# Optimization experiments

Measured on AMD Instinct MI355X. Metric: run time of the kernel, lower is better.

## Reference

```python
import jax, jax.numpy as jnp
import numpy as np

D_MODEL = 1024
N_HEADS = 16
D_HEAD = D_MODEL // N_HEADS
D_FF = 4096
EPS = 1e-5
NEG = -1e10


def setup_inputs() -> dict:
    key = jax.random.key(0)
    ks = jax.random.split(key, 16)
    s = 0.02
    x = jax.random.normal(ks[0], (4, 1024, D_MODEL), dtype=jnp.float32)
    mask = jnp.ones((4, 1, 1, 1024), dtype=jnp.int32)
    return {
        "x": x,
        "mask": mask,
        "Wq": jax.random.normal(ks[1], (D_MODEL, D_MODEL), jnp.float32) * s,
        "Wk": jax.random.normal(ks[2], (D_MODEL, D_MODEL), jnp.float32) * s,
        "Wv": jax.random.normal(ks[3], (D_MODEL, D_MODEL), jnp.float32) * s,
        "Wp": jax.random.normal(ks[4], (D_MODEL, D_MODEL), jnp.float32) * s,
        "bp": jnp.zeros((D_MODEL,), jnp.float32),
        "W1": jax.random.normal(ks[5], (D_MODEL, D_FF), jnp.float32) * s,
        "b1": jnp.zeros((D_FF,), jnp.float32),
        "W2": jax.random.normal(ks[6], (D_FF, D_MODEL), jnp.float32) * s,
        "b2": jnp.zeros((D_MODEL,), jnp.float32),
        "g1": jnp.ones((D_MODEL,), jnp.float32),
        "be1": jnp.zeros((D_MODEL,), jnp.float32),
        "g2": jnp.ones((D_MODEL,), jnp.float32),
        "be2": jnp.zeros((D_MODEL,), jnp.float32),
    }


def _layer_norm(x, g, b):
    mu = jnp.mean(x, axis=-1, keepdims=True)
    var = jnp.mean(jnp.square(x - mu), axis=-1, keepdims=True)
    return (x - mu) * jax.lax.rsqrt(var + EPS) * g + b


def _mha(x, mask, Wq, Wk, Wv, Wp, bp):
    B, L, _ = x.shape
    q = (x @ Wq).reshape(B, L, N_HEADS, D_HEAD).transpose(0, 2, 1, 3)  # (B,H,L,dh)
    k = (x @ Wk).reshape(B, L, N_HEADS, D_HEAD).transpose(0, 2, 1, 3)
    v = (x @ Wv).reshape(B, L, N_HEADS, D_HEAD).transpose(0, 2, 1, 3)
    scores = jnp.einsum('bhqd,bhkd->bhqk', q, k) / jnp.sqrt(jnp.float32(D_HEAD))
    scores = jnp.where(mask == 0, NEG, scores)
    attn = jax.nn.softmax(scores, axis=-1)
    heads = jnp.einsum('bhqk,bhkd->bhqd', attn, v)  # (B,H,L,dh)
    heads = heads.transpose(0, 2, 1, 3).reshape(B, L, D_MODEL)
    return heads @ Wp + bp


def reference(x, mask, Wq, Wk, Wv, Wp, bp, W1, b1, W2, b2, g1, be1, g2, be2):
    # Post-norm residual sublayers (dropout inactive at inference)
    attn_out = _mha(x, mask, Wq, Wk, Wv, Wp, bp)
    h = _layer_norm(x + attn_out, g1, be1)
    ff = jax.nn.relu(h @ W1 + b1) @ W2 + b2
    out = _layer_norm(h + ff, g2, be2)
    return out
```

## Files before the change

kernel.cpp:

```cpp
#include <hip/hip_runtime.h>
#include <hip/hip_bf16.h>

typedef __attribute__((ext_vector_type(8))) short short8;
typedef __attribute__((ext_vector_type(4))) short short4v;
typedef __attribute__((ext_vector_type(4))) float float4v;

static __device__ __forceinline__ float b2f(short s) {
    return __builtin_bit_cast(float, ((unsigned)(unsigned short)s) << 16);
}
static __device__ __forceinline__ short f2b(float f) {
    unsigned x = __builtin_bit_cast(unsigned, f);
    unsigned r = (x + 0x7fffu + ((x >> 16) & 1u)) >> 16;
    return (short)r;
}
static __device__ __forceinline__ void gload_lds16(const short* g, short* l) {
    __builtin_amdgcn_global_load_lds(
        (const __attribute__((address_space(1))) void*)g,
        (__attribute__((address_space(3))) void*)l, 16, 0, 0);
}

__global__ __launch_bounds__(256) void cvt_k(const float* __restrict__ in,
                                             short* __restrict__ out)
{
    const size_t i = ((size_t)blockIdx.x * 256 + threadIdx.x) * 4;
    const float4v v = *(const float4v*)&in[i];
    short4v s;
#pragma unroll
    for (int j = 0; j < 4; j++) s[j] = f2b(v[j]);
    *(short4v*)&out[i] = s;
}

__global__ __launch_bounds__(256) void transpose_cvt_k(const float* __restrict__ in,
                                                       short* __restrict__ out,
                                                       int R, int C)
{
    __shared__ float tile[64][65];
    const int tx = threadIdx.x;
    const int r0 = blockIdx.y * 64, c0 = blockIdx.x * 64;
    const int lr = tx >> 4, lc = (tx & 15) * 4;
#pragma unroll
    for (int p = 0; p < 4; p++) {
        const float4v v = *(const float4v*)&in[(size_t)(r0 + lr + p * 16) * C + c0 + lc];
#pragma unroll
        for (int j = 0; j < 4; j++) tile[lr + p * 16][lc + j] = v[j];
    }
    __syncthreads();
    const int oc = tx >> 3, orr = (tx & 7) * 8;
#pragma unroll
    for (int p = 0; p < 2; p++) {
        const int c = oc + p * 32;
        short8 pk;
#pragma unroll
        for (int j = 0; j < 8; j++) pk[j] = f2b(tile[orr + j][c]);
        *(short8*)&out[(size_t)(c0 + c) * R + r0 + orr] = pk;
    }
}

#define BK 32
template<int MODE, int BM>
__global__ __launch_bounds__(256) void gemm_bt(const short* __restrict__ X,
                                               const short* __restrict__ Wt,
                                               short* __restrict__ out,
                                               const float* __restrict__ bias,
                                               const short* __restrict__ res,
                                               int M, int N, int K)
{
    constexpr int MI = BM / 32;
    constexpr int WM = BM / 2;
    __shared__ short As[BM * BK];
    __shared__ short Bs[128 * BK];
    const int tid = threadIdx.x;
    const int wave = tid >> 6, lane = tid & 63;
    const int quad = lane >> 4, l16 = lane & 15;
    const int m0 = blockIdx.y * BM, n0 = blockIdx.x * 128;
    const int wm = (wave >> 1) * WM, wn = (wave & 1) * 64;

    const int srow = tid >> 2, scol = (tid & 3) * 8;
    const short* gA0 = X  + (size_t)(m0 + srow) * K + scol;
    const short* gA1 = X  + (size_t)(m0 + srow + 64) * K + scol;
    const short* gB0 = Wt + (size_t)(n0 + srow) * K + scol;
    const short* gB1 = Wt + (size_t)(n0 + srow + 64) * K + scol;
    short* lA0 = As + tid * 8;
    short* lA1 = As + (tid + 256) * 8;
    short* lB0 = Bs + tid * 8;
    short* lB1 = Bs + (tid + 256) * 8;

    float4v acc[MI][4] = {};

    for (int k0 = 0; k0 < K; k0 += BK) {
        gload_lds16(gA0 + k0, lA0);
        if (BM == 128) gload_lds16(gA1 + k0, lA1);
        gload_lds16(gB0 + k0, lB0);
        gload_lds16(gB1 + k0, lB1);
        __syncthreads();
        short8 af[MI], bfr[4];
#pragma unroll
        for (int i = 0; i < MI; i++) af[i]  = *(const short8*)&As[(wm + i * 16 + l16) * BK + quad * 8];
#pragma unroll
        for (int i = 0; i < 4; i++)  bfr[i] = *(const short8*)&Bs[(wn + i * 16 + l16) * BK + quad * 8];
#pragma unroll
        for (int mi = 0; mi < MI; mi++)
#pragma unroll
            for (int ni = 0; ni < 4; ni++)
                acc[mi][ni] = __builtin_amdgcn_mfma_f32_16x16x32_bf16(af[mi], bfr[ni], acc[mi][ni], 0, 0, 0);
        __syncthreads();
    }

#pragma unroll
    for (int mi = 0; mi < MI; mi++) {
#pragma unroll
        for (int ni = 0; ni < 4; ni++) {
            const int gn = n0 + wn + ni * 16 + l16;
            const float bv = (MODE == 2 || MODE == 3) ? bias[gn] : 0.0f;
#pragma unroll
            for (int r = 0; r < 4; r++) {
                const int gm = m0 + wm + mi * 16 + quad * 4 + r;
                float v = acc[mi][ni][r];
                if (MODE == 4) {
                    const int s = gn >> 10;
                    const int n = gn & 1023;
                    const int hh = n >> 6, d = n & 63;
                    const size_t bh16 = (size_t)((gm >> 10) * 16 + hh) << 16;
                    const size_t base = (size_t)s << 22;
                    if (s == 0)      out[base + bh16 + ((size_t)(gm & 1023) << 6) + d] = f2b(v * 0.125f);
                    else if (s == 1) out[base + bh16 + ((size_t)(gm & 1023) << 6) + d] = f2b(v);
                    else             out[base + bh16 + ((size_t)d << 10) + (gm & 1023)] = f2b(v);
                } else if (MODE == 2) {
                    v += bv;
                    v = fmaxf(v, 0.0f);
                    out[(size_t)gm * N + gn] = f2b(v);
                } else {
                    v += bv + b2f(res[(size_t)gm * N + gn]);
                    out[(size_t)gm * N + gn] = f2b(v);
                }
            }
        }
    }
}

__global__ __launch_bounds__(256) void attn_k(const short* __restrict__ Qb,
                                              const short* __restrict__ Kb,
                                              const short* __restrict__ Vt,
                                              const int* __restrict__ mask,
                                              short* __restrict__ heads)
{
    __shared__ short Kl[2][64 * 32];
    __shared__ short Vl[2][64 * 32];
    __shared__ short P[4][16 * 72];
    const int bh = blockIdx.x, qb = blockIdx.y;
    const int b = bh >> 4, h = bh & 15;
    const int tid = threadIdx.x, wave = tid >> 6, lane = tid & 63;
    const int quad = lane >> 4, l16 = lane & 15;
    const int qbase = qb * 64 + wave * 16;
    const short* Qp = Qb + ((size_t)bh << 16) + (size_t)qbase * 64;
    const short* Kp = Kb + ((size_t)bh << 16);
    const short* Vp = Vt + ((size_t)bh << 16);
    const int* mp = mask + (b << 10);

    const short8 bq0 = *(const short8*)&Qp[l16 * 64 + quad * 8];
    const short8 bq1 = *(const short8*)&Qp[l16 * 64 + 32 + quad * 8];

    float rs = 0.0f;
    float4v o[4] = {};
    short* myP = &P[wave][0];

    const int srow = tid >> 2, sc8 = (tid & 3) * 8;

    for (int kc = 0; kc < 1024; kc += 64) {
        gload_lds16(Kp + (size_t)(kc + srow) * 64 + sc8,      &Kl[0][tid * 8]);
        gload_lds16(Kp + (size_t)(kc + srow) * 64 + 32 + sc8, &Kl[1][tid * 8]);
        gload_lds16(Vp + (size_t)srow * 1024 + kc + sc8,      &Vl[0][tid * 8]);
        gload_lds16(Vp + (size_t)srow * 1024 + kc + 32 + sc8, &Vl[1][tid * 8]);
        __syncthreads();

        float4v s[4];
#pragma unroll
        for (int kt = 0; kt < 4; kt++) {
            s[kt] = (float4v){};
            const short8 ka = *(const short8*)&Kl[0][(kt * 16 + l16) * 32 + quad * 8];
            s[kt] = __builtin_amdgcn_mfma_f32_16x16x32_bf16(ka, bq0, s[kt], 0, 0, 0);
            const short8 kb = *(const short8*)&Kl[1][(kt * 16 + l16) * 32 + quad * 8];
            s[kt] = __builtin_amdgcn_mfma_f32_16x16x32_bf16(kb, bq1, s[kt], 0, 0, 0);
        }
#pragma unroll
        for (int kt = 0; kt < 4; kt++) {
            const int4 mv = *(const int4*)&mp[kc + kt * 16 + quad * 4];
            float p0 = mv.x ? __expf(fminf(s[kt][0], 30.f)) : 0.f;
            float p1 = mv.y ? __expf(fminf(s[kt][1], 30.f)) : 0.f;
            float p2 = mv.z ? __expf(fminf(s[kt][2], 30.f)) : 0.f;
            float p3 = mv.w ? __expf(fminf(s[kt][3], 30.f)) : 0.f;
            rs += (p0 + p1) + (p2 + p3);
            short4v w;
            w[0] = f2b(p0); w[1] = f2b(p1); w[2] = f2b(p2); w[3] = f2b(p3);
            *(short4v*)&myP[l16 * 72 + kt * 16 + quad * 4] = w;
        }
        const short8 bp0 = *(const short8*)&myP[l16 * 72 + quad * 8];
        const short8 bp1 = *(const short8*)&myP[l16 * 72 + 32 + quad * 8];
#pragma unroll
        for (int dt = 0; dt < 4; dt++) {
            const short8 va = *(const short8*)&Vl[0][(dt * 16 + l16) * 32 + quad * 8];
            o[dt] = __builtin_amdgcn_mfma_f32_16x16x32_bf16(va, bp0, o[dt], 0, 0, 0);
            const short8 vb = *(const short8*)&Vl[1][(dt * 16 + l16) * 32 + quad * 8];
            o[dt] = __builtin_amdgcn_mfma_f32_16x16x32_bf16(vb, bp1, o[dt], 0, 0, 0);
        }
        __syncthreads();
    }

    rs += __shfl_xor(rs, 16);
    rs += __shfl_xor(rs, 32);
    const float inv = 1.0f / fmaxf(rs, 1e-20f);
    const int gq = qbase + l16;
#pragma unroll
    for (int dt = 0; dt < 4; dt++) {
        short4v w;
#pragma unroll
        for (int r = 0; r < 4; r++) w[r] = f2b(o[dt][r] * inv);
        *(short4v*)&heads[((size_t)(b * 1024 + gq) << 10) + h * 64 + dt * 16 + quad * 4] = w;
    }
}

template<bool F32OUT>
__global__ __launch_bounds__(256) void ln_k(const short* __restrict__ in,
                                            const float* __restrict__ g,
                                            const float* __restrict__ be,
                                            short* __restrict__ outb,
                                            float* __restrict__ outf)
{
    __shared__ float red[8];
    const int row = blockIdx.x, tid = threadIdx.x;
    const short* p = in + ((size_t)row << 10);
    float v[4];
#pragma unroll
    for (int i = 0; i < 4; i++) v[i] = b2f(p[tid + i * 256]);
    float s = v[0] + v[1] + v[2] + v[3];
#pragma unroll
    for (int off = 32; off; off >>= 1) s += __shfl_xor(s, off);
    if ((tid & 63) == 0) red[tid >> 6] = s;
    __syncthreads();
    const float mu = (red[0] + red[1] + red[2] + red[3]) * (1.0f / 1024.0f);
    float vs = 0.f;
#pragma unroll
    for (int i = 0; i < 4; i++) { const float d = v[i] - mu; vs += d * d; }
#pragma unroll
    for (int off = 32; off; off >>= 1) vs += __shfl_xor(vs, off);
    if ((tid & 63) == 0) red[4 + (tid >> 6)] = vs;
    __syncthreads();
    const float rstd = rsqrtf((red[4] + red[5] + red[6] + red[7]) * (1.0f / 1024.0f) + 1e-5f);
#pragma unroll
    for (int i = 0; i < 4; i++) {
        const int c = tid + i * 256;
        const float r = (v[i] - mu) * rstd * g[c] + be[c];
        if (F32OUT) outf[((size_t)row << 10) + c] = r;
        else        outb[((size_t)row << 10) + c] = f2b(r);
    }
}

extern "C" void kernel_launch(void* const* d_in, const int* in_sizes, int n_in,
                              void* d_out, int out_size, void* d_ws, size_t ws_size,
                              hipStream_t stream)
{
    const float* x   = (const float*)d_in[0];
    const int*   mk  = (const int*)d_in[1];
    const float* Wq  = (const float*)d_in[2];
    const float* Wk  = (const float*)d_in[3];
    const float* Wv  = (const float*)d_in[4];
    const float* Wp  = (const float*)d_in[5];
    const float* bp  = (const float*)d_in[6];
    const float* W1  = (const float*)d_in[7];
    const float* b1  = (const float*)d_in[8];
    const float* W2  = (const float*)d_in[9];
    const float* b2  = (const float*)d_in[10];
    const float* g1  = (const float*)d_in[11];
    const float* be1 = (const float*)d_in[12];
    const float* g2  = (const float*)d_in[13];
    const float* be2 = (const float*)d_in[14];
    float* out = (float*)d_out;

    char* ws = (char*)d_ws;
    const size_t MB = (size_t)1 << 20;
    short* xb     = (short*)(ws + 0 * MB);
    short* WqkvT  = (short*)(ws + 8 * MB);
    short* WpT    = (short*)(ws + 14 * MB);
    short* W1T    = (short*)(ws + 16 * MB);
    short* W2T    = (short*)(ws + 24 * MB);
    short* Qb     = (short*)(ws + 32 * MB);
    short* Kb     = (short*)(ws + 40 * MB);
    short* Vt     = (short*)(ws + 48 * MB);
    short* hd     = (short*)(ws + 56 * MB);
    short* u      = (short*)(ws + 32 * MB);
    short* hpre   = (short*)(ws + 64 * MB);
    short* hbuf   = (short*)(ws + 72 * MB);

    const dim3 blk(256);

    cvt_k<<<dim3(4096), blk, 0, stream>>>(x, xb);

    transpose_cvt_k<<<dim3(16, 16), blk, 0, stream>>>(Wq, WqkvT, 1024, 1024);
    transpose_cvt_k<<<dim3(16, 16), blk, 0, stream>>>(Wk, WqkvT + (1 << 20), 1024, 1024);
    transpose_cvt_k<<<dim3(16, 16), blk, 0, stream>>>(Wv, WqkvT + (2 << 20), 1024, 1024);
    transpose_cvt_k<<<dim3(16, 16), blk, 0, stream>>>(Wp, WpT, 1024, 1024);
    transpose_cvt_k<<<dim3(64, 16), blk, 0, stream>>>(W1, W1T, 1024, 4096);
    transpose_cvt_k<<<dim3(16, 64), blk, 0, stream>>>(W2, W2T, 4096, 1024);

    gemm_bt<4, 128><<<dim3(24, 32), blk, 0, stream>>>(xb, WqkvT, Qb, nullptr, nullptr, 4096, 3072, 1024);

    attn_k<<<dim3(64, 16), blk, 0, stream>>>(Qb, Kb, Vt, mk, hd);

    gemm_bt<3, 64><<<dim3(8, 64), blk, 0, stream>>>(hd, WpT, hpre, bp, xb, 4096, 1024, 1024);

    ln_k<false><<<dim3(4096), blk, 0, stream>>>(hpre, g1, be1, hbuf, nullptr);

    gemm_bt<2, 128><<<dim3(32, 32), blk, 0, stream>>>(hbuf, W1T, u, b1, nullptr, 4096, 4096, 1024);

    gemm_bt<3, 64><<<dim3(8, 64), blk, 0, stream>>>(u, W2T, hpre, b2, hbuf, 4096, 1024, 4096);

    ln_k<true><<<dim3(4096), blk, 0, stream>>>(hpre, g2, be2, nullptr, out);
}
```

Baseline: 383.9 us.

## Double the GEMM K-step to 64 and add a BN template parameter

The GEMM main loop now loads a 64-wide K slice per iteration into two 32-wide LDS halves. This halves the number of barrier pairs and loop iterations and gives more MFMA work between syncs. A BN template parameter is added, and the two N=1024 GEMMs switch to 64x64 tiles with twice as many blocks to improve occupancy and CU fill. The cost is more LDS per block and a smaller tile size with less reuse for those two GEMMs.

```diff
diff --git a/kernel.cpp b/kernel.cpp
--- a/kernel.cpp
+++ b/kernel.cpp
@@ -56,8 +56,7 @@
     }
 }
 
-#define BK 32
-template<int MODE, int BM>
+template<int MODE, int BM, int BN>
 __global__ __launch_bounds__(256) void gemm_bt(const short* __restrict__ X,
                                                const short* __restrict__ Wt,
                                                short* __restrict__ out,
@@ -65,51 +64,53 @@
                                                const short* __restrict__ res,
                                                int M, int N, int K)
 {
-    constexpr int MI = BM / 32;
-    constexpr int WM = BM / 2;
-    __shared__ short As[BM * BK];
-    __shared__ short Bs[128 * BK];
+    constexpr int MI = BM / 32, NI = BN / 32;
+    __shared__ short As[2][BM * 32];
+    __shared__ short Bs[2][BN * 32];
     const int tid = threadIdx.x;
     const int wave = tid >> 6, lane = tid & 63;
     const int quad = lane >> 4, l16 = lane & 15;
-    const int m0 = blockIdx.y * BM, n0 = blockIdx.x * 128;
-    const int wm = (wave >> 1) * WM, wn = (wave & 1) * 64;
-
-    const int srow = tid >> 2, scol = (tid & 3) * 8;
-    const short* gA0 = X  + (size_t)(m0 + srow) * K + scol;
-    const short* gA1 = X  + (size_t)(m0 + srow + 64) * K + scol;
-    const short* gB0 = Wt + (size_t)(n0 + srow) * K + scol;
-    const short* gB1 = Wt + (size_t)(n0 + srow + 64) * K + scol;
-    short* lA0 = As + tid * 8;
-    short* lA1 = As + (tid + 256) * 8;
-    short* lB0 = Bs + tid * 8;
-    short* lB1 = Bs + (tid + 256) * 8;
-
-    float4v acc[MI][4] = {};
-
-    for (int k0 = 0; k0 < K; k0 += BK) {
-        gload_lds16(gA0 + k0, lA0);
-        if (BM == 128) gload_lds16(gA1 + k0, lA1);
-        gload_lds16(gB0 + k0, lB0);
-        gload_lds16(gB1 + k0, lB1);
+    const int m0 = blockIdx.y * BM, n0 = blockIdx.x * BN;
+    const int wm = (wave >> 1) * (BM / 2), wn = (wave & 1) * (BN / 2);
+
+    const int srow = tid >> 2, sc8 = (tid & 3) * 8;
+
+    float4v acc[MI][NI] = {};
+
+    for (int k0 = 0; k0 < K; k0 += 64) {
+#pragma unroll
+        for (int c = 0; c < BM / 64; c++) {
+            const short* g = X + (size_t)(m0 + c * 64 + srow) * K + k0 + sc8;
+            gload_lds16(g,      &As[0][(c * 256 + tid) * 8]);
+            gload_lds16(g + 32, &As[1][(c * 256 + tid) * 8]);
+        }
+#pragma unroll
+        for (int c = 0; c < BN / 64; c++) {
+            const short* g = Wt + (size_t)(n0 + c * 64 + srow) * K + k0 + sc8;
+            gload_lds16(g,      &Bs[0][(c * 256 + tid) * 8]);
+            gload_lds16(g + 32, &Bs[1][(c * 256 + tid) * 8]);
+        }
         __syncthreads();
-        short8 af[MI], bfr[4];
-#pragma unroll
-        for (int i = 0; i < MI; i++) af[i]  = *(const short8*)&As[(wm + i * 16 + l16) * BK + quad * 8];
-#pragma unroll
-        for (int i = 0; i < 4; i++)  bfr[i] = *(const short8*)&Bs[(wn + i * 16 + l16) * BK + quad * 8];
-#pragma unroll
-        for (int mi = 0; mi < MI; mi++)
-#pragma unroll
-            for (int ni = 0; ni < 4; ni++)
-                acc[mi][ni] = __builtin_amdgcn_mfma_f32_16x16x32_bf16(af[mi], bfr[ni], acc[mi][ni], 0, 0, 0);
+#pragma unroll
+        for (int h = 0; h < 2; h++) {
+            short8 af[MI], bf[NI];
+#pragma unroll
+            for (int i = 0; i < MI; i++) af[i] = *(const short8*)&As[h][(wm + i * 16 + l16) * 32 + quad * 8];
+#pragma unroll
+            for (int i = 0; i < NI; i++) bf[i] = *(const short8*)&Bs[h][(wn + i * 16 + l16) * 32 + quad * 8];
+#pragma unroll
+            for (int mi = 0; mi < MI; mi++)
+#pragma unroll
+                for (int ni = 0; ni < NI; ni++)
+                    acc[mi][ni] = __builtin_amdgcn_mfma_f32_16x16x32_bf16(af[mi], bf[ni], acc[mi][ni], 0, 0, 0);
+        }
         __syncthreads();
     }
 
 #pragma unroll
     for (int mi = 0; mi < MI; mi++) {
 #pragma unroll
-        for (int ni = 0; ni < 4; ni++) {
+        for (int ni = 0; ni < NI; ni++) {
             const int gn = n0 + wn + ni * 16 + l16;
             const float bv = (MODE == 2 || MODE == 3) ? bias[gn] : 0.0f;
 #pragma unroll
@@ -302,17 +303,17 @@
     transpose_cvt_k<<<dim3(64, 16), blk, 0, stream>>>(W1, W1T, 1024, 4096);
     transpose_cvt_k<<<dim3(16, 64), blk, 0, stream>>>(W2, W2T, 4096, 1024);
 
-    gemm_bt<4, 128><<<dim3(24, 32), blk, 0, stream>>>(xb, WqkvT, Qb, nullptr, nullptr, 4096, 3072, 1024);
+    gemm_bt<4, 128, 128><<<dim3(24, 32), blk, 0, stream>>>(xb, WqkvT, Qb, nullptr, nullptr, 4096, 3072, 1024);
 
     attn_k<<<dim3(64, 16), blk, 0, stream>>>(Qb, Kb, Vt, mk, hd);
 
-    gemm_bt<3, 64><<<dim3(8, 64), blk, 0, stream>>>(hd, WpT, hpre, bp, xb, 4096, 1024, 1024);
+    gemm_bt<3, 64, 64><<<dim3(16, 64), blk, 0, stream>>>(hd, WpT, hpre, bp, xb, 4096, 1024, 1024);
 
     ln_k<false><<<dim3(4096), blk, 0, stream>>>(hpre, g1, be1, hbuf, nullptr);
 
-    gemm_bt<2, 128><<<dim3(32, 32), blk, 0, stream>>>(hbuf, W1T, u, b1, nullptr, 4096, 4096, 1024);
-
-    gemm_bt<3, 64><<<dim3(8, 64), blk, 0, stream>>>(u, W2T, hpre, b2, hbuf, 4096, 1024, 4096);
+    gemm_bt<2, 128, 128><<<dim3(32, 32), blk, 0, stream>>>(hbuf, W1T, u, b1, nullptr, 4096, 4096, 1024);
+
+    gemm_bt<3, 64, 64><<<dim3(16, 64), blk, 0, stream>>>(u, W2T, hpre, b2, hbuf, 4096, 1024, 4096);
 
     ln_k<true><<<dim3(4096), blk, 0, stream>>>(hpre, g2, be2, nullptr, out);
 }
```

Result: faster. 354.3 us (-7.7%).
